# Optimization experiments

Hardware: AMD Instinct MI355X
Metric: run time of the kernel (lower is better)

Reference implementation:

```python
import jax, jax.numpy as jnp
import numpy as np

B = 256
N_VERTS = 10475
N_JOINTS = 55  # 1 root + 21 body + jaw + 2 eyes + 2*15 hands
NUM_BETAS = 10
NUM_EXPR = 10
POSE_BASIS = (N_JOINTS - 1) * 9  # 486
# SMPL-X kinematic tree (parent index per joint, root = -1)
PARENTS = np.array([-1,0,0,0,1,2,3,4,5,6,7,8,9,9,9,12,13,14,16,17,18,19,15,15,15,
                    20,25,26,20,28,29,20,31,32,20,34,35,20,37,38,
                    21,40,41,21,43,44,21,46,47,21,49,50,21,52,53], dtype=np.int64)


def _rodrigues(aa):
    # axis-angle [..., 3] -> rotation matrix [..., 3, 3]
    angle = jnp.linalg.norm(aa, axis=-1, keepdims=True) + 1e-8
    axis = aa / angle
    x, y, z = axis[..., 0], axis[..., 1], axis[..., 2]
    zero = jnp.zeros_like(x)
    K = jnp.stack([zero, -z, y, z, zero, -x, -y, x, zero], axis=-1).reshape(aa.shape[:-1] + (3, 3))
    s = jnp.sin(angle)[..., None]
    c = jnp.cos(angle)[..., None]
    I = jnp.eye(3, dtype=aa.dtype)
    return I + s * K + (1.0 - c) * (K @ K)


def setup_inputs() -> dict:
    key = jax.random.key(0)
    ks = jax.random.split(key, 16)
    def rots(k, nj, scale=0.2):
        aa = jax.random.normal(k, (B, nj, 3), dtype=jnp.float32) * scale
        return _rodrigues(aa)
    inp = {
        'world_rot': rots(ks[0], 1, 0.5),
        'world_tsl': jax.random.normal(ks[1], (B, 3), dtype=jnp.float32),
        'body_shape': jax.random.normal(ks[2], (B, NUM_BETAS), dtype=jnp.float32),
        'body_pose': rots(ks[3], 21),
        'left_hand_pose': rots(ks[4], 15),
        'right_hand_pose': rots(ks[5], 15),
        'expr_shape': jax.random.normal(ks[6], (B, NUM_EXPR), dtype=jnp.float32),
        'jaw_pose': rots(ks[7], 1),
        'leye_pose': rots(ks[8], 1),
        'reye_pose': rots(ks[9], 1),
        # model buffers (synthetic, SMPL-X-sized)
        'v_template': jax.random.normal(ks[10], (N_VERTS, 3), dtype=jnp.float32) * 0.3,
        'shapedirs': jax.random.normal(ks[11], (N_VERTS, 3, NUM_BETAS), dtype=jnp.float32) * 0.01,
        'expr_dirs': jax.random.normal(ks[12], (N_VERTS, 3, NUM_EXPR), dtype=jnp.float32) * 0.01,
        'posedirs': jax.random.normal(ks[13], (POSE_BASIS, N_VERTS * 3), dtype=jnp.float32) * 0.01,
        'J_regressor': jax.nn.softmax(jax.random.normal(ks[14], (N_JOINTS, N_VERTS), dtype=jnp.float32) * 4.0, axis=-1),
        'lbs_weights': jax.nn.softmax(jax.random.normal(ks[15], (N_VERTS, N_JOINTS), dtype=jnp.float32) * 4.0, axis=-1),
    }
    return inp


def _lbs(world_rot, world_tsl, body_shape, body_pose, left_hand_pose, right_hand_pose,
         expr_shape, jaw_pose, leye_pose, reye_pose,
         v_template, shapedirs, expr_dirs, posedirs, J_regressor, lbs_weights):
    dtype = v_template.dtype
    # full pose: [B, 55, 3, 3]
    full_pose = jnp.concatenate([world_rot, body_pose, jaw_pose, leye_pose, reye_pose,
                                 left_hand_pose, right_hand_pose], axis=1)
    b = full_pose.shape[0]
    # shape + expression blendshapes
    v_shaped = v_template[None] + jnp.einsum('bk,nck->bnc', body_shape, shapedirs) \
               + jnp.einsum('bk,nck->bnc', expr_shape, expr_dirs)
    # rest-pose joints [B, J, 3]
    joints = jnp.einsum('jn,bnc->bjc', J_regressor, v_shaped)
    # pose blendshapes
    ident = jnp.eye(3, dtype=dtype)
    pose_feature = (full_pose[:, 1:] - ident).reshape(b, POSE_BASIS)
    v_posed = v_shaped + (pose_feature @ posedirs).reshape(b, N_VERTS, 3)
    # relative joint locations w.r.t. parent
    rel_joints = joints.at[:, 1:].add(-joints[:, PARENTS[1:]])
    # local 4x4 transforms [B, J, 4, 4]
    top = jnp.concatenate([full_pose, rel_joints[..., None]], axis=-1)  # [B,J,3,4]
    bottom = jnp.broadcast_to(jnp.array([0., 0., 0., 1.], dtype=dtype), (b, N_JOINTS, 1, 4))
    T = jnp.concatenate([top, bottom], axis=2)
    # kinematic chain recurrence (small fixed joint count -> unrolled)
    chain = [T[:, 0]]
    for i in range(1, N_JOINTS):
        chain.append(chain[PARENTS[i]] @ T[:, i])
    A = jnp.stack(chain, axis=1)  # [B, J, 4, 4]
    posed_joints = A[..., :3, 3]
    # remove rest-pose joint offset so A maps rest -> posed
    t_corr = posed_joints - jnp.einsum('bjkl,bjl->bjk', A[..., :3, :3], joints)
    A_rel = A.at[..., :3, 3].set(t_corr)
    # linear blend skinning: per-vertex transform [B, N, 4, 4]
    T_vert = jnp.einsum('nj,bjkl->bnkl', lbs_weights, A_rel)
    verts = jnp.einsum('bnkl,bnl->bnk', T_vert[..., :3, :3], v_posed) + T_vert[..., :3, 3]
    verts = verts + world_tsl[:, None]
    joints_out = posed_joints + world_tsl[:, None]
    return verts, joints_out


def reference(world_rot, world_tsl, body_shape, body_pose, left_hand_pose, right_hand_pose,
              expr_shape, jaw_pose, leye_pose, reye_pose,
              v_template, shapedirs, expr_dirs, posedirs, J_regressor, lbs_weights):
    return _lbs(world_rot, world_tsl, body_shape, body_pose, left_hand_pose, right_hand_pose,
                expr_shape, jaw_pose, leye_pose, reye_pose,
                v_template, shapedirs, expr_dirs, posedirs, J_regressor, lbs_weights)
```

## Files before the change

kernel.cpp:

```cpp
#include <hip/hip_runtime.h>
#include <stdint.h>

#define BATCH 256
#define NV 10475
#define NVP 10496
#define NJ 55
#define PB 486
#define KS 506
#define VC (NV*3)
#define KP 512
#define BKC 32
#define NCHUNK 16
#define BN 64
#define JCH 8
#define JCHUNK 1312

typedef short bf16x8 __attribute__((ext_vector_type(8)));
typedef float f32x4  __attribute__((ext_vector_type(4)));

__constant__ int c_parents[NJ] = {
  -1,0,0,0,1,2,3,4,5,6,7,8,9,9,9,12,13,14,16,17,18,19,15,15,15,
  20,25,26,20,28,29,20,31,32,20,34,35,20,37,38,21,40,41,21,43,44,
  21,46,47,21,49,50,21,52,53};

__constant__ int c_depth[NJ] = {
  0,1,1,1,2,2,2,3,3,3,4,4,4,4,4,5,5,5,6,6,7,7,6,6,6,
  8,9,10,8,9,10,8,9,10,8,9,10,8,9,10,
  8,9,10,8,9,10,8,9,10,8,9,10,8,9,10};

__device__ __forceinline__ unsigned short f2bf(float x){
  uint32_t u = __float_as_uint(x);
  uint32_t r = (u + 0x7fffu + ((u >> 16) & 1u)) >> 16;
  return (unsigned short)r;
}
__device__ __forceinline__ float bf2f(unsigned short h){
  return __uint_as_float(((uint32_t)h) << 16);
}

__device__ __forceinline__ const float* pose_src(int j, int b,
    const float* wrot, const float* bpose, const float* jaw, const float* leye,
    const float* reye, const float* lhand, const float* rhand) {
  if (j==0)  return wrot  + b*9;
  if (j<=21) return bpose + (b*21 + (j-1))*9;
  if (j==22) return jaw   + b*9;
  if (j==23) return leye  + b*9;
  if (j==24) return reye  + b*9;
  if (j<=39) return lhand + (b*15 + (j-25))*9;
  return rhand + (b*15 + (j-40))*9;
}

#define LWB_BLOCKS 2624
#define PF_BLOCKS  BATCH
#define JS_BLOCKS  (JCH*NJ)
#define FRONT_BLOCKS (LWB_BLOCKS + PF_BLOCKS + JS_BLOCKS)

__global__ __launch_bounds__(256) void k_front(
    const float* __restrict__ lw,
    const float* __restrict__ bpose, const float* __restrict__ jaw,
    const float* __restrict__ leye, const float* __restrict__ reye,
    const float* __restrict__ lhand, const float* __restrict__ rhand,
    const float* __restrict__ bs, const float* __restrict__ es,
    const float* __restrict__ jreg, const float* __restrict__ sd,
    const float* __restrict__ ed, const float* __restrict__ vt,
    unsigned short* __restrict__ lwb, unsigned short* __restrict__ pfb,
    float* __restrict__ part) {
  const int bid = blockIdx.x, t = threadIdx.x;
  if (bid < LWB_BLOCKS) {
    int idx = bid*256 + t;
    int n = idx >> 6, j = idx & 63;
    float v = (n < NV && j < NJ) ? lw[(size_t)n*NJ + j] : 0.f;
    unsigned short hi = f2bf(v);
    float lo = v - bf2f(hi);
    lwb[idx] = hi;
    lwb[(size_t)NVP*64 + idx] = f2bf(lo);
  } else if (bid < LWB_BLOCKS + PF_BLOCKS) {
    int b = bid - LWB_BLOCKS;
    #pragma unroll
    for (int half=0; half<2; half++){
      int tt = t + half*256;
      unsigned short o = 0;
      if (tt < PB){
        int jj = tt/9, rc = tt - jj*9;
        const float* rs = pose_src(jj+1, b, nullptr, bpose, jaw, leye, reye, lhand, rhand);
        float v = rs[rc];
        if (rc==0 || rc==4 || rc==8) v -= 1.0f;
        o = f2bf(v);
      } else if (tt < 496){
        o = f2bf(bs[b*10 + (tt-486)]);
      } else if (tt < KS){
        o = f2bf(es[b*10 + (tt-496)]);
      }
      pfb[(size_t)b*KP + tt] = o;
    }
  } else {
    int idx = bid - (LWB_BLOCKS + PF_BLOCKS);
    int ch = idx & 7, j = idx >> 3;
    float acc[63];
    #pragma unroll
    for (int s=0;s<63;s++) acc[s]=0.f;
    int n0 = ch*JCHUNK, nend = min(n0+JCHUNK, NV);
    for (int n = n0 + t; n < nend; n += 256){
      float w = jreg[(size_t)j*NV + n];
      const float* sp = sd + (size_t)n*30;
      const float* ep = ed + (size_t)n*30;
      const float* vp = vt + (size_t)n*3;
      #pragma unroll
      for (int c=0;c<3;c++){
        #pragma unroll
        for (int q=0;q<10;q++){
          acc[c*21+q]    += w*sp[c*10+q];
          acc[c*21+10+q] += w*ep[c*10+q];
        }
        acc[c*21+20] += w*vp[c];
      }
    }
    #pragma unroll
    for (int s=0;s<63;s++){
      float a = acc[s];
      #pragma unroll
      for (int d=32; d>=1; d>>=1) a += __shfl_xor(a,d);
      acc[s]=a;
    }
    __shared__ float red[4][63];
    int w = t>>6, l = t&63;
    if (l==0){
      #pragma unroll
      for (int s=0;s<63;s++) red[w][s]=acc[s];
    }
    __syncthreads();
    if (t < 63){
      float a = red[0][t]+red[1][t]+red[2][t]+red[3][t];
      part[((size_t)j*JCH+ch)*63 + t] = a;
    }
  }
}

__global__ __launch_bounds__(256) void k_mid(
    const float* __restrict__ part, const float* __restrict__ bs,
    const float* __restrict__ es,
    const float* __restrict__ wrot, const float* __restrict__ bpose,
    const float* __restrict__ jaw, const float* __restrict__ leye,
    const float* __restrict__ reye, const float* __restrict__ lhand,
    const float* __restrict__ rhand, const float* __restrict__ wtsl,
    unsigned short* __restrict__ arelb, float* __restrict__ jout) {
  __shared__ float jlds[NJ*3];
  const int b = blockIdx.x, t = threadIdx.x;
  if (t < NJ*3){
    int j = t/3, c = t - j*3;
    float S[21];
    #pragma unroll
    for (int q=0;q<21;q++) S[q]=0.f;
    for (int ch=0; ch<JCH; ch++){
      const float* p = part + ((size_t)j*JCH+ch)*63 + c*21;
      #pragma unroll
      for (int q=0;q<21;q++) S[q] += p[q];
    }
    float a = S[20];
    #pragma unroll
    for (int q=0;q<10;q++) a += S[q]*bs[b*10+q] + S[10+q]*es[b*10+q];
    jlds[t] = a;
  }
  __syncthreads();
  if (t >= 64) return;
  const int j = t;
  const bool act = (j < NJ);

  float R[9] = {1.f,0.f,0.f, 0.f,1.f,0.f, 0.f,0.f,1.f};
  if (act){
    const float* rs = pose_src(j, b, wrot, bpose, jaw, leye, reye, lhand, rhand);
    #pragma unroll
    for (int i=0;i<9;i++) R[i]=rs[i];
  }
  float jx=0.f, jy=0.f, jz=0.f;
  if (act){ jx=jlds[j*3+0]; jy=jlds[j*3+1]; jz=jlds[j*3+2]; }
  int par = act ? c_parents[j] : 0;
  if (par < 0) par = 0;
  float px = __shfl(jx, par), py = __shfl(jy, par), pz = __shfl(jz, par);
  float t0, t1, t2;
  if (j == 0){ t0=jx; t1=jy; t2=jz; }
  else       { t0=jx-px; t1=jy-py; t2=jz-pz; }

  float M[12];
  #pragma unroll
  for (int r=0;r<3;r++){
    M[r*4+0]=R[r*3+0]; M[r*4+1]=R[r*3+1]; M[r*4+2]=R[r*3+2]; M[r*4+3]= (r==0?t0:(r==1?t1:t2));
  }
  int dep = act ? c_depth[j] : 99;

  #pragma unroll
  for (int L=1; L<=10; L++){
    float pm[12];
    #pragma unroll
    for (int i=0;i<12;i++) pm[i] = __shfl(M[i], par);
    if (dep == L){
      #pragma unroll
      for (int r=0;r<3;r++){
        float p0=pm[r*4+0], p1=pm[r*4+1], p2=pm[r*4+2], p3=pm[r*4+3];
        M[r*4+0] = p0*R[0]+p1*R[3]+p2*R[6];
        M[r*4+1] = p0*R[1]+p1*R[4]+p2*R[7];
        M[r*4+2] = p0*R[2]+p1*R[5]+p2*R[8];
        M[r*4+3] = p0*t0 + p1*t1 + p2*t2 + p3;
      }
    }
  }

  float wx=wtsl[b*3+0], wy=wtsl[b*3+1], wz=wtsl[b*3+2];
  if (act){
    jout[((size_t)b*NJ+j)*3+0] = M[3]  + wx;
    jout[((size_t)b*NJ+j)*3+1] = M[7]  + wy;
    jout[((size_t)b*NJ+j)*3+2] = M[11] + wz;
  }
  float A[12];
  #pragma unroll
  for (int r=0;r<3;r++){
    A[r*4+0]=M[r*4+0]; A[r*4+1]=M[r*4+1]; A[r*4+2]=M[r*4+2];
    A[r*4+3]=M[r*4+3] - (M[r*4+0]*jx + M[r*4+1]*jy + M[r*4+2]*jz);
  }
  unsigned short* ah = arelb + (size_t)(b*2+0)*16*64;
  unsigned short* al = arelb + (size_t)(b*2+1)*16*64;
  #pragma unroll
  for (int e=0;e<16;e++){
    float v = (e < 12 && act) ? A[e] : 0.f;
    unsigned short hi = f2bf(v);
    float lo = v - bf2f(hi);
    ah[e*64 + j] = hi;
    al[e*64 + j] = f2bf(lo);
  }
}

__global__ __launch_bounds__(256, 2) void k_vposed(
    const float* __restrict__ pd, const float* __restrict__ sd,
    const float* __restrict__ ed, const float* __restrict__ vt,
    const unsigned short* __restrict__ pfb, float* __restrict__ vsh) {
  const int tid  = threadIdx.x;
  const int w    = tid >> 6, lane = tid & 63;
  const int m16  = lane & 15, quad = lane >> 4;
  const int col0 = blockIdx.x * BN;

  f32x4 acc[4][4];
  #pragma unroll
  for (int i=0;i<4;i++)
    #pragma unroll
    for (int j=0;j<4;j++) acc[i][j] = (f32x4){0.f,0.f,0.f,0.f};

  int bcol[4];
  #pragma unroll
  for (int ni=0;ni<4;ni++) bcol[ni] = min(col0 + ni*16 + m16, VC-1);

  const unsigned short* pfa = pfb + (size_t)(w*64 + m16)*KP + quad*8;

  #pragma unroll 2
  for (int c=0; c<15; c++){
    const int k0 = c*BKC;
    bf16x8 a[4];
    #pragma unroll
    for (int mi=0;mi<4;mi++)
      a[mi] = *((const bf16x8*)(pfa + (size_t)mi*16*KP + k0));
    union { bf16x8 v; unsigned short s[8]; } bb[4];
    #pragma unroll
    for (int ni=0;ni<4;ni++){
      #pragma unroll
      for (int j=0;j<8;j++){
        int kk = k0 + quad*8 + j;
        bb[ni].s[j] = f2bf(pd[(size_t)kk*VC + bcol[ni]]);
      }
    }
    #pragma unroll
    for (int mi=0;mi<4;mi++)
      #pragma unroll
      for (int ni=0;ni<4;ni++)
        acc[mi][ni] = __builtin_amdgcn_mfma_f32_16x16x32_bf16(
                          a[mi], bb[ni].v, acc[mi][ni], 0, 0, 0);
  }
  {
    const int k0 = 15*BKC;
    bf16x8 a[4];
    #pragma unroll
    for (int mi=0;mi<4;mi++)
      a[mi] = *((const bf16x8*)(pfa + (size_t)mi*16*KP + k0));
    union { bf16x8 v; unsigned short s[8]; } bb[4];
    #pragma unroll
    for (int ni=0;ni<4;ni++){
      int n3 = bcol[ni]/3, c3 = bcol[ni] - n3*3;
      const float* sp = sd + (size_t)n3*30 + c3*10;
      const float* ep = ed + (size_t)n3*30 + c3*10;
      #pragma unroll
      for (int j=0;j<8;j++){
        int kk = k0 + quad*8 + j;
        float f = 0.f;
        if (kk < PB)      f = pd[(size_t)kk*VC + bcol[ni]];
        else if (kk < KS){
          int q = kk - PB;
          f = (q < 10) ? sp[q] : ep[q-10];
        }
        bb[ni].s[j] = f2bf(f);
      }
    }
    #pragma unroll
    for (int mi=0;mi<4;mi++)
      #pragma unroll
      for (int ni=0;ni<4;ni++)
        acc[mi][ni] = __builtin_amdgcn_mfma_f32_16x16x32_bf16(
                          a[mi], bb[ni].v, acc[mi][ni], 0, 0, 0);
  }
  #pragma unroll
  for (int mi=0;mi<4;mi++){
    int rbase = w*64 + mi*16 + quad*4;
    #pragma unroll
    for (int ni=0;ni<4;ni++){
      int col = col0 + ni*16 + m16;
      if (col < VC){
        float vtc = vt[col];
        #pragma unroll
        for (int r=0;r<4;r++)
          vsh[(size_t)(rbase + r)*VC + col] = acc[mi][ni][r] + vtc;
      }
    }
  }
}

__global__ __launch_bounds__(256) void k_verts(
    const unsigned short* __restrict__ lwb, const unsigned short* __restrict__ arelb,
    const float* __restrict__ wtsl, float* __restrict__ out) {
  __shared__ float sT[4*816];
  const int tid = threadIdx.x, w = tid >> 6, lane = tid & 63;
  const int m16 = lane & 15, quad = lane >> 4;
  const int n0 = blockIdx.x*64;
  const int b0 = blockIdx.y*16;
  float* myT = &sT[w*816];

  bf16x8 lwh[4][2], lwl[4][2];
  #pragma unroll
  for (int vt4=0; vt4<4; vt4++){
    int row = n0 + vt4*16 + m16;
    #pragma unroll
    for (int kc=0;kc<2;kc++){
      lwh[vt4][kc] = *((const bf16x8*)(lwb + (size_t)row*64 + kc*32 + quad*8));
      lwl[vt4][kc] = *((const bf16x8*)(lwb + (size_t)NVP*64 + (size_t)row*64 + kc*32 + quad*8));
    }
  }
  const int nA = n0 + lane;
  const bool okA = (nA < NV);

  for (int bi=0; bi<4; bi++){
    const int b = b0 + w*4 + bi;
    bf16x8 ah[2], al[2];
    #pragma unroll
    for (int kc=0;kc<2;kc++){
      ah[kc] = *((const bf16x8*)(arelb + ((size_t)(b*2+0)*16 + m16)*64 + kc*32 + quad*8));
      al[kc] = *((const bf16x8*)(arelb + ((size_t)(b*2+1)*16 + m16)*64 + kc*32 + quad*8));
    }
    const float* vp = out + ((size_t)b*NV + nA)*3;
    float vx = okA ? vp[0] : 0.f;
    float vy = okA ? vp[1] : 0.f;
    float vz = okA ? vp[2] : 0.f;

    f32x4 acc[4];
    #pragma unroll
    for (int vt4=0; vt4<4; vt4++) acc[vt4] = (f32x4){0.f,0.f,0.f,0.f};
    #pragma unroll
    for (int vt4=0; vt4<4; vt4++){
      #pragma unroll
      for (int kc=0;kc<2;kc++){
        acc[vt4] = __builtin_amdgcn_mfma_f32_16x16x32_bf16(ah[kc], lwh[vt4][kc], acc[vt4], 0,0,0);
        acc[vt4] = __builtin_amdgcn_mfma_f32_16x16x32_bf16(al[kc], lwh[vt4][kc], acc[vt4], 0,0,0);
        acc[vt4] = __builtin_amdgcn_mfma_f32_16x16x32_bf16(ah[kc], lwl[vt4][kc], acc[vt4], 0,0,0);
      }
    }
    #pragma unroll
    for (int vt4=0; vt4<4; vt4++){
      if (quad < 3){
        #pragma unroll
        for (int r=0;r<4;r++)
          myT[(quad*4 + r)*68 + vt4*16 + m16] = acc[vt4][r];
      }
    }
    float T[12];
    #pragma unroll
    for (int e=0;e<12;e++) T[e] = myT[e*68 + lane];
    if (okA){
      float tx=wtsl[b*3+0], ty=wtsl[b*3+1], tz=wtsl[b*3+2];
      float* op = out + ((size_t)b*NV + nA)*3;
      op[0] = T[0]*vx + T[1]*vy + T[2] *vz + T[3]  + tx;
      op[1] = T[4]*vx + T[5]*vy + T[6] *vz + T[7]  + ty;
      op[2] = T[8]*vx + T[9]*vy + T[10]*vz + T[11] + tz;
    }
  }
}

extern "C" void kernel_launch(void* const* d_in, const int* in_sizes, int n_in,
                              void* d_out, int out_size, void* d_ws, size_t ws_size,
                              hipStream_t stream) {
  const float* wrot   = (const float*)d_in[0];
  const float* wtsl   = (const float*)d_in[1];
  const float* bshape = (const float*)d_in[2];
  const float* bpose  = (const float*)d_in[3];
  const float* lhand  = (const float*)d_in[4];
  const float* rhand  = (const float*)d_in[5];
  const float* eshape = (const float*)d_in[6];
  const float* jaw    = (const float*)d_in[7];
  const float* leye   = (const float*)d_in[8];
  const float* reye   = (const float*)d_in[9];
  const float* vt     = (const float*)d_in[10];
  const float* sd     = (const float*)d_in[11];
  const float* ed     = (const float*)d_in[12];
  const float* pd     = (const float*)d_in[13];
  const float* jreg   = (const float*)d_in[14];
  const float* lw     = (const float*)d_in[15];
  float* out = (float*)d_out;

  float* vsh  = out;
  float* jout = out + (size_t)BATCH*NV*3;

  float* ws   = (float*)d_ws;
  float* part = ws;
  unsigned short* pfb   = (unsigned short*)(part + (size_t)NJ*JCH*63);
  unsigned short* lwb   = pfb + (size_t)BATCH*KP;
  unsigned short* arelb = lwb + (size_t)2*NVP*64;

  k_front <<<FRONT_BLOCKS, 256, 0, stream>>>(lw, bpose, jaw, leye, reye,
                                             lhand, rhand, bshape, eshape,
                                             jreg, sd, ed, vt, lwb, pfb, part);
  k_mid   <<<BATCH, 256, 0, stream>>>(part, bshape, eshape, wrot, bpose, jaw,
                                      leye, reye, lhand, rhand, wtsl, arelb, jout);
  k_vposed<<<(VC+BN-1)/BN, 256, 0, stream>>>(pd, sd, ed, vt, pfb, vsh);
  k_verts <<<dim3(NVP/64, 16), 256, 0, stream>>>(lwb, arelb, wtsl, out);
}
```

Measured before the change: 246.8 us.

## Stage posedirs tiles through double-buffered LDS with vectorized loads in k_vposed

The B operand (posedirs columns) was read with scalar strided global loads, each thread issuing 32 separate loads per chunk, and every wave in the block fetched the same values. Now each thread issues coalesced float4 loads, converts them to bf16 and writes a padded, double-buffered shared-memory tile, with the next chunk's loads issued before the MFMAs. Waves then read B fragments from LDS. This adds LDS traffic and a __syncthreads per chunk, and removes the occupancy hint from launch_bounds.

```diff
diff --git a/kernel.cpp b/kernel.cpp
--- a/kernel.cpp
+++ b/kernel.cpp
@@ -12,6 +12,7 @@
 #define BKC 32
 #define NCHUNK 16
 #define BN 64
+#define PADC 70
 #define JCH 8
 #define JCHUNK 1312
 
@@ -228,14 +229,20 @@
   }
 }
 
-__global__ __launch_bounds__(256, 2) void k_vposed(
+__global__ __launch_bounds__(256) void k_vposed(
     const float* __restrict__ pd, const float* __restrict__ sd,
     const float* __restrict__ ed, const float* __restrict__ vt,
     const unsigned short* __restrict__ pfb, float* __restrict__ vsh) {
+  __shared__ unsigned short bt[2][32*PADC];
   const int tid  = threadIdx.x;
   const int w    = tid >> 6, lane = tid & 63;
   const int m16  = lane & 15, quad = lane >> 4;
   const int col0 = blockIdx.x * BN;
+  const bool tail = (col0 + BN > VC);
+
+  const int sf4 = tid & 15;
+  const int sr  = tid >> 4;
+  const int scol = col0 + sf4*4;
 
   f32x4 acc[4][4];
   #pragma unroll
@@ -243,14 +250,62 @@
     #pragma unroll
     for (int j=0;j<4;j++) acc[i][j] = (f32x4){0.f,0.f,0.f,0.f};
 
-  int bcol[4];
-  #pragma unroll
-  for (int ni=0;ni<4;ni++) bcol[ni] = min(col0 + ni*16 + m16, VC-1);
-
   const unsigned short* pfa = pfb + (size_t)(w*64 + m16)*KP + quad*8;
 
-  #pragma unroll 2
-  for (int c=0; c<15; c++){
+  auto LD = [&](int kk)->f32x4 {
+    if (!tail) return *((const f32x4*)(pd + (size_t)kk*VC + scol));
+    f32x4 r;
+    #pragma unroll
+    for (int i=0;i<4;i++){
+      int cc = scol + i;
+      r[i] = (cc < VC) ? pd[(size_t)kk*VC + cc] : 0.f;
+    }
+    return r;
+  };
+  auto STORE4 = [&](unsigned short* buf, int row, const f32x4& v){
+    uint32_t p0 = (uint32_t)f2bf(v[0]) | ((uint32_t)f2bf(v[1]) << 16);
+    uint32_t p1 = (uint32_t)f2bf(v[2]) | ((uint32_t)f2bf(v[3]) << 16);
+    uint32_t* q = (uint32_t*)(buf + row*PADC + sf4*4);
+    q[0] = p0; q[1] = p1;
+  };
+
+  f32x4 ra = LD(0*BKC + sr), rb = LD(0*BKC + sr + 16);
+
+  for (int c = 0; c < NCHUNK; ++c){
+    unsigned short* buf = &bt[c & 1][0];
+    if (c < 15){
+      STORE4(buf, sr,      ra);
+      STORE4(buf, sr + 16, rb);
+      if (c + 1 < 15){
+        ra = LD((c+1)*BKC + sr);
+        rb = LD((c+1)*BKC + sr + 16);
+      }
+    } else {
+      int colL = tid & 63, rg = tid >> 6;
+      int colG = col0 + colL;
+      if (colG < VC){
+        int n3 = colG/3, c3 = colG - n3*3;
+        const float* sp = sd + (size_t)n3*30 + c3*10;
+        const float* ep = ed + (size_t)n3*30 + c3*10;
+        #pragma unroll
+        for (int rr = 0; rr < 8; rr++){
+          int r = rg*8 + rr;
+          int kk = 480 + r;
+          float f = 0.f;
+          if (kk < PB)      f = pd[(size_t)kk*VC + colG];
+          else if (kk < KS){
+            int q = kk - PB;
+            f = (q < 10) ? sp[q] : ep[q-10];
+          }
+          buf[r*PADC + colL] = f2bf(f);
+        }
+      } else {
+        #pragma unroll
+        for (int rr = 0; rr < 8; rr++) buf[(rg*8+rr)*PADC + colL] = 0;
+      }
+    }
+    __syncthreads();
+
     const int k0 = c*BKC;
     bf16x8 a[4];
     #pragma unroll
@@ -260,41 +315,8 @@
     #pragma unroll
     for (int ni=0;ni<4;ni++){
       #pragma unroll
-      for (int j=0;j<8;j++){
-        int kk = k0 + quad*8 + j;
-        bb[ni].s[j] = f2bf(pd[(size_t)kk*VC + bcol[ni]]);
-      }
-    }
-    #pragma unroll
-    for (int mi=0;mi<4;mi++)
-      #pragma unroll
-      for (int ni=0;ni<4;ni++)
-        acc[mi][ni] = __builtin_amdgcn_mfma_f32_16x16x32_bf16(
-                          a[mi], bb[ni].v, acc[mi][ni], 0, 0, 0);
-  }
-  {
-    const int k0 = 15*BKC;
-    bf16x8 a[4];
-    #pragma unroll
-    for (int mi=0;mi<4;mi++)
-      a[mi] = *((const bf16x8*)(pfa + (size_t)mi*16*KP + k0));
-    union { bf16x8 v; unsigned short s[8]; } bb[4];
-    #pragma unroll
-    for (int ni=0;ni<4;ni++){
-      int n3 = bcol[ni]/3, c3 = bcol[ni] - n3*3;
-      const float* sp = sd + (size_t)n3*30 + c3*10;
-      const float* ep = ed + (size_t)n3*30 + c3*10;
-      #pragma unroll
-      for (int j=0;j<8;j++){
-        int kk = k0 + quad*8 + j;
-        float f = 0.f;
-        if (kk < PB)      f = pd[(size_t)kk*VC + bcol[ni]];
-        else if (kk < KS){
-          int q = kk - PB;
-          f = (q < 10) ? sp[q] : ep[q-10];
-        }
-        bb[ni].s[j] = f2bf(f);
-      }
+      for (int j=0;j<8;j++)
+        bb[ni].s[j] = buf[(quad*8 + j)*PADC + ni*16 + m16];
     }
     #pragma unroll
     for (int mi=0;mi<4;mi++)
@@ -424,5 +446,5 @@
   k_mid   <<<BATCH, 256, 0, stream>>>(part, bshape, eshape, wrot, bpose, jaw,
                                       leye, reye, lhand, rhand, wtsl, arelb, jout);
   k_vposed<<<(VC+BN-1)/BN, 256, 0, stream>>>(pd, sd, ed, vt, pfb, vsh);
-  k_verts <<<dim3(NVP/64, 16), 256, 0, stream>>>(lwb, arelb, wtsl, out);
-}
+  k_verts <<<dim3(NVP/64, BATCH/16), 256, 0, stream>>>(lwb, arelb, wtsl, out);
+}
```

Result: faster. 240.5 us (-2.6%).
